# Optimization experiments

Measured on AMD Instinct MI355X. Metric: run time of the kernel, lower is better.

The kernel has to match this reference:

```python
import jax, jax.numpy as jnp
import numpy as np

MODEL_DIM = 1024
NUM_HEADS = 16
HEAD_DIM = MODEL_DIM // NUM_HEADS
EPS = 1e-12
CHUNK = 128  # chunk size for the linear-attention recurrence


def setup_inputs() -> dict:
    key = jax.random.key(0)
    kx, kq, kk, kv, ko = jax.random.split(key, 5)
    b, l = 4, 4096
    x = jax.random.normal(kx, (b, l, MODEL_DIM), dtype=jnp.float32)
    # nn.Linear weights, init std=0.02, no bias; torch Linear computes x @ W.T
    Wq = 0.02 * jax.random.normal(kq, (MODEL_DIM, MODEL_DIM), dtype=jnp.float32)
    Wk = 0.02 * jax.random.normal(kk, (MODEL_DIM, MODEL_DIM), dtype=jnp.float32)
    Wv = 0.02 * jax.random.normal(kv, (MODEL_DIM, MODEL_DIM), dtype=jnp.float32)
    Wo = 0.02 * jax.random.normal(ko, (MODEL_DIM, MODEL_DIM), dtype=jnp.float32)
    return {"x": x, "Wq": Wq, "Wk": Wk, "Wv": Wv, "Wo": Wo}


def _pos_elu(t):
    # feature_map = F.elu(x) + 1
    return jax.nn.elu(t) + 1.0


def _linear_attention(q, k, v):
    # q,k,v: (b,h,l,d) with feature map already applied.
    # Causal linear attention: out_t = (q_t . sum_{s<=t} k_s v_s^T) / (q_t . sum_{s<=t} k_s) + EPS
    # Chunked recurrence over the (d,d) KV state avoids the (b,h,l,d,d) cumsum.
    b, h, l, d = q.shape
    nc = l // CHUNK
    qc = jnp.moveaxis(q.reshape(b, h, nc, CHUNK, d), 2, 0)  # (nc,b,h,C,d)
    kc = jnp.moveaxis(k.reshape(b, h, nc, CHUNK, d), 2, 0)
    vc = jnp.moveaxis(v.reshape(b, h, nc, CHUNK, d), 2, 0)
    mask = jnp.tril(jnp.ones((CHUNK, CHUNK), dtype=q.dtype))  # causal within chunk

    def step(carry, inp):
        S, z = carry  # S:(b,h,d,d) running sum k v^T; z:(b,h,d) running sum k
        qb, kb, vb = inp  # (b,h,C,d)
        scores = jnp.einsum('bhcd,bhsd->bhcs', qb, kb) * mask  # (b,h,C,C)
        num = jnp.einsum('bhcd,bhde->bhce', qb, S) + jnp.einsum('bhcs,bhse->bhce', scores, vb)
        den = jnp.einsum('bhcd,bhd->bhc', qb, z) + scores.sum(-1)  # (b,h,C)
        out = num / den[..., None] + EPS  # NOTE: eps added after division, as in source
        S = S + jnp.einsum('bhsd,bhse->bhde', kb, vb)
        z = z + kb.sum(axis=2)
        return (S, z), out

    S0 = jnp.zeros((b, h, d, d), dtype=q.dtype)
    z0 = jnp.zeros((b, h, d), dtype=q.dtype)
    _, outs = jax.lax.scan(step, (S0, z0), (qc, kc, vc))  # (nc,b,h,C,d)
    # -> (b, l, h, d)
    return jnp.moveaxis(outs, 0, 1).transpose(0, 3, 1, 2, 4).reshape(b, h * 0 + l // l, 0, 0) if False else outs


def reference(x, Wq, Wk, Wv, Wo):
    b, l, D = x.shape
    h, d = NUM_HEADS, HEAD_DIM
    # projections (torch Linear: x @ W.T), split heads -> (b,h,l,d)
    q = (x @ Wq.T).reshape(b, l, h, d).transpose(0, 2, 1, 3)
    k = (x @ Wk.T).reshape(b, l, h, d).transpose(0, 2, 1, 3)
    v = (x @ Wv.T).reshape(b, l, h, d).transpose(0, 2, 1, 3)
    q = _pos_elu(q)
    k = _pos_elu(k)
    outs = _linear_attention(q, k, v)  # (nc,b,h,C,d)
    nc = l // CHUNK
    # (nc,b,h,C,d) -> (b,nc,C,h,d) -> (b,l,D)  (matches transpose(1,2).view in torch)
    attn = outs.transpose(1, 0, 3, 2, 4).reshape(b, l, D)
    return attn @ Wo.T
```

## Files before the change

### kernel.cpp

```cpp
#include <hip/hip_runtime.h>
#include <stdint.h>

typedef float f32x4 __attribute__((ext_vector_type(4)));
typedef __bf16 bf16x8 __attribute__((ext_vector_type(8)));
typedef unsigned short u16x8 __attribute__((ext_vector_type(8)));

#define DEV __device__ __forceinline__

DEV unsigned short f2bf(float f) {
  unsigned int u = __float_as_uint(f);
  unsigned int r = (u + 0x7FFFu + ((u >> 16) & 1u)) >> 16;
  return (unsigned short)r;
}
DEV float b2f(unsigned short h) { return __uint_as_float(((unsigned int)h) << 16); }

DEV void gload16(const void* g, void* l) {
  __builtin_amdgcn_global_load_lds((__attribute__((address_space(1))) void*)(g),
                                   (__attribute__((address_space(3))) void*)(l), 16, 0, 0);
}

__global__ void cast_bf16_kernel(const float* __restrict__ in,
                                 unsigned short* __restrict__ out, int n8) {
  int i = blockIdx.x * 256 + threadIdx.x;
  if (i >= n8) return;
  const float4* p = (const float4*)in + (size_t)i * 2;
  float4 a = p[0], b = p[1];
  u16x8 o;
  o[0] = f2bf(a.x); o[1] = f2bf(a.y); o[2] = f2bf(a.z); o[3] = f2bf(a.w);
  o[4] = f2bf(b.x); o[5] = f2bf(b.y); o[6] = f2bf(b.z); o[7] = f2bf(b.w);
  ((u16x8*)out)[i] = o;
}

__global__ void cast_w4(const float* __restrict__ Wq, const float* __restrict__ Wk,
                        const float* __restrict__ Wv, const float* __restrict__ Wo,
                        unsigned short* __restrict__ wqkv, unsigned short* __restrict__ wo) {
  int i = blockIdx.x * 256 + threadIdx.x;
  int sel = i >> 17, j = i & 131071;
  const float* src = (sel == 0) ? Wq : (sel == 1) ? Wk : (sel == 2) ? Wv : Wo;
  unsigned short* dst = (sel < 3) ? (wqkv + (size_t)sel * 1048576) : wo;
  const float4* p = (const float4*)src + (size_t)j * 2;
  float4 a = p[0], b = p[1];
  u16x8 o;
  o[0] = f2bf(a.x); o[1] = f2bf(a.y); o[2] = f2bf(a.z); o[3] = f2bf(a.w);
  o[4] = f2bf(b.x); o[5] = f2bf(b.y); o[6] = f2bf(b.z); o[7] = f2bf(b.w);
  ((u16x8*)dst)[j] = o;
}

template<int MODE>
__global__ __launch_bounds__(256, 2) void gemm_bt(
    const unsigned short* __restrict__ A, const unsigned short* __restrict__ Bw,
    void* __restrict__ out0, unsigned short* __restrict__ qp,
    unsigned short* __restrict__ kp, unsigned short* __restrict__ vp,
    int K, int N, int nTn)
{
  __shared__ unsigned short sA[128 * 64];
  __shared__ unsigned short sB[128 * 64];
  int t = threadIdx.x, w = t >> 6, lane = t & 63, fr = lane & 15, fq = lane >> 4;
  int nwg = gridDim.x, cpx = nwg >> 3;
  int bid = (blockIdx.x & 7) * cpx + (blockIdx.x >> 3);
  int bm = bid / nTn, bn = bid % nTn;
  int wm = w >> 1, wn = w & 1;

  f32x4 acc[4][4];
  f32x4 z4 = {0.f, 0.f, 0.f, 0.f};
#pragma unroll
  for (int mi = 0; mi < 4; ++mi)
#pragma unroll
    for (int ni = 0; ni < 4; ++ni) acc[mi][ni] = z4;

  for (int k0 = 0; k0 < K; k0 += 64) {
#pragma unroll
    for (int i = 0; i < 4; ++i) {
      int p = (i * 4 + w) * 64 + lane;
      int r = p >> 3;
      int c8 = (p & 7) ^ (r & 7);
      gload16(A + (size_t)(bm * 128 + r) * K + k0 + c8 * 8, &sA[(i * 4 + w) * 512]);
      gload16(Bw + (size_t)(bn * 128 + r) * K + k0 + c8 * 8, &sB[(i * 4 + w) * 512]);
    }
    __syncthreads();
#pragma unroll
    for (int ks = 0; ks < 2; ++ks) {
      bf16x8 af[4], bg[4];
#pragma unroll
      for (int mi = 0; mi < 4; ++mi) {
        int r = wm * 64 + mi * 16 + fr;
        int c8 = (ks * 4 + fq) ^ (r & 7);
        af[mi] = *(const bf16x8*)&sA[(r * 8 + c8) * 8];
      }
#pragma unroll
      for (int ni = 0; ni < 4; ++ni) {
        int r = wn * 64 + ni * 16 + fr;
        int c8 = (ks * 4 + fq) ^ (r & 7);
        bg[ni] = *(const bf16x8*)&sB[(r * 8 + c8) * 8];
      }
#pragma unroll
      for (int mi = 0; mi < 4; ++mi)
#pragma unroll
        for (int ni = 0; ni < 4; ++ni)
          acc[mi][ni] = __builtin_amdgcn_mfma_f32_16x16x32_bf16(af[mi], bg[ni], acc[mi][ni], 0, 0, 0);
    }
    __syncthreads();
  }

  if (MODE == 0) {
    float* O = (float*)out0;
#pragma unroll
    for (int mi = 0; mi < 4; ++mi)
#pragma unroll
      for (int ni = 0; ni < 4; ++ni)
#pragma unroll
        for (int j = 0; j < 4; ++j) {
          int m = bm * 128 + wm * 64 + mi * 16 + fq * 4 + j;
          int n = bn * 128 + wn * 64 + ni * 16 + fr;
          O[(size_t)m * N + n] = acc[mi][ni][j];
        }
  } else {
    int tsel = (bn * 128) >> 10;
    unsigned short* base = (tsel == 0) ? qp : ((tsel == 1) ? kp : vp);
#pragma unroll
    for (int mi = 0; mi < 4; ++mi)
#pragma unroll
      for (int ni = 0; ni < 4; ++ni)
#pragma unroll
        for (int j = 0; j < 4; ++j) {
          int m = bm * 128 + wm * 64 + mi * 16 + fq * 4 + j;
          int n = bn * 128 + wn * 64 + ni * 16 + fr;
          int col1 = n & 1023;
          int h = col1 >> 6, d = col1 & 63;
          int b = m >> 12, l = m & 4095;
          float v = acc[mi][ni][j];
          if (tsel < 2) v = (v > 0.f) ? (v + 1.f) : __expf(v);
          base[(((size_t)(b * 16 + h)) * 4096 + l) * 64 + d] = f2bf(v);
        }
  }
}

__global__ __launch_bounds__(256) void chunk_state(
    const unsigned short* __restrict__ kb, const unsigned short* __restrict__ vb,
    float* __restrict__ Sbuf, float* __restrict__ zbuf)
{
  __shared__ unsigned short kT[64 * 136];
  __shared__ unsigned short vT[64 * 136];
  int t = threadIdx.x, w = t >> 6, lane = t & 63, fr = lane & 15, fq = lane >> 4;
  int bh = blockIdx.x >> 5, c = blockIdx.x & 31;
  size_t base = ((size_t)bh * 4096 + (size_t)c * 128) * 64;

  int s = t >> 1, d0 = (t & 1) * 32;
  const unsigned short* kpp = kb + base + (size_t)s * 64 + d0;
  const unsigned short* vpp = vb + base + (size_t)s * 64 + d0;
#pragma unroll
  for (int i = 0; i < 4; ++i) {
    u16x8 kr = *(const u16x8*)(kpp + i * 8);
    u16x8 vr = *(const u16x8*)(vpp + i * 8);
#pragma unroll
    for (int j = 0; j < 8; ++j) {
      int d = d0 + i * 8 + j;
      kT[d * 136 + s] = kr[j];
      vT[d * 136 + s] = vr[j];
    }
  }
  __syncthreads();

  f32x4 acc[4];
  f32x4 z4 = {0.f, 0.f, 0.f, 0.f};
#pragma unroll
  for (int n = 0; n < 4; ++n) acc[n] = z4;
#pragma unroll
  for (int ks = 0; ks < 4; ++ks) {
    bf16x8 av = *(const bf16x8*)&vT[(w * 16 + fr) * 136 + ks * 32 + fq * 8];
#pragma unroll
    for (int n = 0; n < 4; ++n) {
      bf16x8 bk = *(const bf16x8*)&kT[(n * 16 + fr) * 136 + ks * 32 + fq * 8];
      acc[n] = __builtin_amdgcn_mfma_f32_16x16x32_bf16(av, bk, acc[n], 0, 0, 0);
    }
  }
  size_t ob = ((size_t)bh * 32 + c) * 4096;
#pragma unroll
  for (int n = 0; n < 4; ++n)
#pragma unroll
    for (int j = 0; j < 4; ++j) {
      int e = w * 16 + fq * 4 + j, d = n * 16 + fr;
      Sbuf[ob + (size_t)e * 64 + d] = acc[n][j];
    }
  if (t < 64) {
    float z = 0.f;
#pragma unroll
    for (int i = 0; i < 16; ++i) {
      u16x8 kr = *(const u16x8*)&kT[t * 136 + i * 8];
#pragma unroll
      for (int j = 0; j < 8; ++j) z += b2f(kr[j]);
    }
    zbuf[((size_t)bh * 32 + c) * 64 + t] = z;
  }
}

__global__ __launch_bounds__(256) void scan_S(
    const float* __restrict__ Sbuf, unsigned short* __restrict__ Spref)
{
  int idx = blockIdx.x * 256 + threadIdx.x;
  int bh = idx >> 12, i = idx & 4095;
  size_t base = (size_t)bh * 32 * 4096 + i;
  float run = 0.f;
#pragma unroll
  for (int c = 0; c < 32; ++c) {
    float v = Sbuf[base + (size_t)c * 4096];
    Spref[base + (size_t)c * 4096] = f2bf(run);
    run += v;
  }
}

__global__ __launch_bounds__(256) void scan_z(
    const float* __restrict__ zbuf, float* __restrict__ zpref)
{
  int idx = blockIdx.x * 256 + threadIdx.x;
  size_t base = (size_t)(idx >> 6) * 32 * 64 + (idx & 63);
  float run = 0.f;
#pragma unroll
  for (int c = 0; c < 32; ++c) {
    float v = zbuf[base + c * 64];
    zpref[base + c * 64] = run;
    run += v;
  }
}

__global__ __launch_bounds__(256, 2) void chunk_out(
    const unsigned short* __restrict__ qb, const unsigned short* __restrict__ kb,
    const unsigned short* __restrict__ vb, const unsigned short* __restrict__ Spref,
    const float* __restrict__ zpref, unsigned short* __restrict__ attn)
{
  __shared__ unsigned short sq[128 * 64];
  __shared__ unsigned short skv[128 * 64];
  __shared__ unsigned short ss[128 * 128];
  __shared__ unsigned short sS[80 * 64];
  int t = threadIdx.x, w = t >> 6, lane = t & 63, fr = lane & 15, fq = lane >> 4;
  int bh = blockIdx.x >> 5, c = blockIdx.x & 31;
  size_t qkbase = ((size_t)bh * 4096 + (size_t)c * 128) * 64;
  size_t sbase = ((size_t)bh * 32 + c) * 4096;

  u16x8 vreg[4];
#pragma unroll
  for (int i = 0; i < 4; ++i)
    vreg[i] = *(const u16x8*)(vb + qkbase + (size_t)(t * 4 + i) * 8);

#pragma unroll
  for (int i = 0; i < 4; ++i) {
    int p = t * 4 + i, r = p >> 3, c8 = p & 7;
    int sw = (r * 8 + (c8 ^ (r & 7))) * 8;
    *(u16x8*)&sq[sw] = *(const u16x8*)(qb + qkbase + (size_t)p * 8);
    *(u16x8*)&skv[sw] = *(const u16x8*)(kb + qkbase + (size_t)p * 8);
  }
#pragma unroll
  for (int i = 0; i < 2; ++i) {
    int p = t * 2 + i, e = p >> 3, c8 = p & 7;
    *(u16x8*)&sS[(e * 8 + (c8 ^ (e & 7))) * 8] = *(const u16x8*)(Spref + sbase + (size_t)p * 8);
  }
  if (t < 64) sS[64 * 64 + t] = f2bf(zpref[((size_t)bh * 32 + c) * 64 + t]);
  {
    unsigned int* zz = (unsigned int*)&sS[65 * 64];
    for (int i = t; i < 480; i += 256) zz[i] = 0u;
  }
  __syncthreads();

  int rowbase = w * 32;
  bf16x8 aq[2][2];
#pragma unroll
  for (int mi = 0; mi < 2; ++mi)
#pragma unroll
    for (int kt = 0; kt < 2; ++kt) {
      int r = rowbase + mi * 16 + fr;
      int c8 = (kt * 4 + fq) ^ (r & 7);
      aq[mi][kt] = *(const bf16x8*)&sq[(r * 8 + c8) * 8];
    }

  f32x4 accs[2][8];
  f32x4 z4 = {0.f, 0.f, 0.f, 0.f};
#pragma unroll
  for (int mi = 0; mi < 2; ++mi)
#pragma unroll
    for (int ni = 0; ni < 8; ++ni) accs[mi][ni] = z4;

#pragma unroll
  for (int ni = 0; ni < 8; ++ni)
#pragma unroll
    for (int kt = 0; kt < 2; ++kt) {
      int r = ni * 16 + fr;
      int c8 = (kt * 4 + fq) ^ (r & 7);
      bf16x8 bk = *(const bf16x8*)&skv[(r * 8 + c8) * 8];
      accs[0][ni] = __builtin_amdgcn_mfma_f32_16x16x32_bf16(aq[0][kt], bk, accs[0][ni], 0, 0, 0);
      accs[1][ni] = __builtin_amdgcn_mfma_f32_16x16x32_bf16(aq[1][kt], bk, accs[1][ni], 0, 0, 0);
    }

  float rs[2][4];
#pragma unroll
  for (int mi = 0; mi < 2; ++mi)
#pragma unroll
    for (int j = 0; j < 4; ++j) {
      int srow = rowbase + mi * 16 + fq * 4 + j;
      float sum = 0.f;
#pragma unroll
      for (int ni = 0; ni < 8; ++ni) {
        int scol = ni * 16 + fr;
        float v = accs[mi][ni][j];
        v = (scol <= srow) ? v : 0.f;
        accs[mi][ni][j] = v;
        sum += v;
      }
#pragma unroll
      for (int msk = 1; msk < 16; msk <<= 1) sum += __shfl_xor(sum, msk, 64);
      rs[mi][j] = sum;
    }
  __syncthreads();

#pragma unroll
  for (int i = 0; i < 4; ++i) {
    int p = t * 4 + i, s = p >> 3, e0g = (p & 7) * 8;
#pragma unroll
    for (int j = 0; j < 8; ++j) {
      int e = e0g + j;
      skv[(e * 16 + ((s >> 3) ^ (e & 15))) * 8 + (s & 7)] = vreg[i][j];
    }
  }
#pragma unroll
  for (int mi = 0; mi < 2; ++mi)
#pragma unroll
    for (int ni = 0; ni < 8; ++ni)
#pragma unroll
      for (int j = 0; j < 4; ++j) {
        int srow = rowbase + mi * 16 + fq * 4 + j;
        int scol = ni * 16 + fr;
        ss[(srow * 16 + ((scol >> 3) ^ (srow & 15))) * 8 + (scol & 7)] = f2bf(accs[mi][ni][j]);
      }
  __syncthreads();

  f32x4 acco[2][4];
  f32x4 accd[2];
#pragma unroll
  for (int mi = 0; mi < 2; ++mi) {
    accd[mi] = z4;
#pragma unroll
    for (int ni = 0; ni < 4; ++ni) acco[mi][ni] = z4;
  }
#pragma unroll
  for (int kt = 0; kt < 2; ++kt) {
#pragma unroll
    for (int ni = 0; ni < 4; ++ni) {
      int r = ni * 16 + fr;
      int c8 = (kt * 4 + fq) ^ (r & 7);
      bf16x8 bS = *(const bf16x8*)&sS[(r * 8 + c8) * 8];
      acco[0][ni] = __builtin_amdgcn_mfma_f32_16x16x32_bf16(aq[0][kt], bS, acco[0][ni], 0, 0, 0);
      acco[1][ni] = __builtin_amdgcn_mfma_f32_16x16x32_bf16(aq[1][kt], bS, acco[1][ni], 0, 0, 0);
    }
    {
      int r = 64 + fr;
      int c8 = (kt * 4 + fq) ^ (r & 7);
      bf16x8 bz = *(const bf16x8*)&sS[(r * 8 + c8) * 8];
      accd[0] = __builtin_amdgcn_mfma_f32_16x16x32_bf16(aq[0][kt], bz, accd[0], 0, 0, 0);
      accd[1] = __builtin_amdgcn_mfma_f32_16x16x32_bf16(aq[1][kt], bz, accd[1], 0, 0, 0);
    }
  }
#pragma unroll
  for (int kt = 0; kt < 4; ++kt) {
    bf16x8 am[2];
#pragma unroll
    for (int mi = 0; mi < 2; ++mi) {
      int r = rowbase + mi * 16 + fr;
      int c8 = (kt * 4 + fq) ^ (r & 15);
      am[mi] = *(const bf16x8*)&ss[(r * 16 + c8) * 8];
    }
#pragma unroll
    for (int ni = 0; ni < 4; ++ni) {
      int r = ni * 16 + fr;
      int c8 = (kt * 4 + fq) ^ (r & 15);
      bf16x8 bv = *(const bf16x8*)&skv[(r * 16 + c8) * 8];
      acco[0][ni] = __builtin_amdgcn_mfma_f32_16x16x32_bf16(am[0], bv, acco[0][ni], 0, 0, 0);
      acco[1][ni] = __builtin_amdgcn_mfma_f32_16x16x32_bf16(am[1], bv, acco[1][ni], 0, 0, 0);
    }
  }

  int b = bh >> 4, h = bh & 15;
#pragma unroll
  for (int mi = 0; mi < 2; ++mi)
#pragma unroll
    for (int j = 0; j < 4; ++j) {
      float den = __shfl(accd[mi][j], (lane & 48), 64) + rs[mi][j];
      float rden = 1.f / den;
      int m = rowbase + mi * 16 + fq * 4 + j;
      size_t rowoff = ((size_t)b * 4096 + (size_t)c * 128 + m) * 1024 + h * 64;
#pragma unroll
      for (int ni = 0; ni < 4; ++ni) {
        int e = ni * 16 + fr;
        float o = acco[mi][ni][j] * rden + 1e-12f;
        attn[rowoff + e] = f2bf(o);
      }
    }
}

extern "C" void kernel_launch(void* const* d_in, const int* in_sizes, int n_in,
                              void* d_out, int out_size, void* d_ws, size_t ws_size,
                              hipStream_t stream) {
  (void)in_sizes; (void)n_in; (void)out_size; (void)ws_size;
  const float* x = (const float*)d_in[0];
  const float* Wq = (const float*)d_in[1];
  const float* Wk = (const float*)d_in[2];
  const float* Wv = (const float*)d_in[3];
  const float* Wo = (const float*)d_in[4];
  char* ws = (char*)d_ws;
  unsigned short* xbf  = (unsigned short*)(ws + 0);
  unsigned short* wqkv = (unsigned short*)(ws + 33554432);
  unsigned short* wo   = (unsigned short*)(ws + 39845888);
  unsigned short* q    = (unsigned short*)(ws + 41943040);
  unsigned short* k    = (unsigned short*)(ws + 75497472);
  unsigned short* v    = (unsigned short*)(ws + 109051904);
  unsigned short* attn = (unsigned short*)(ws + 142606336);
  float* Sbuf          = (float*)(ws + 176160768);
  unsigned short* Spref= (unsigned short*)(ws + 209715200);
  float* zbuf          = (float*)(ws + 226492416);
  float* zpref         = (float*)(ws + 227016704);

  cast_bf16_kernel<<<8192, 256, 0, stream>>>(x, xbf, 2097152);
  cast_w4<<<2048, 256, 0, stream>>>(Wq, Wk, Wv, Wo, wqkv, wo);

  gemm_bt<1><<<3072, 256, 0, stream>>>(xbf, wqkv, nullptr, q, k, v, 1024, 3072, 24);
  chunk_state<<<2048, 256, 0, stream>>>(k, v, Sbuf, zbuf);
  scan_S<<<1024, 256, 0, stream>>>(Sbuf, Spref);
  scan_z<<<16, 256, 0, stream>>>(zbuf, zpref);
  chunk_out<<<2048, 256, 0, stream>>>(q, k, v, Spref, zpref, attn);
  gemm_bt<0><<<1024, 256, 0, stream>>>(attn, wo, d_out, nullptr, nullptr, nullptr, 1024, 1024, 8);
}
```

Baseline: 234.8 us.

## Merge cast and scan kernels, drop XCD remap, widen chunk_out to 512 threads

Fuses the two cast kernels into one launch and the two scan kernels into one launch to cut launch overhead. Removes the XCD-aware block remapping in the GEMM, so tiles are assigned in plain block order. Doubles chunk_out to 512 threads with 16 rows per wave instead of 32, which raises the wave count per block but halves per-wave MFMA work and register use. Dropping the remap may hurt L2 locality on the multi-XCD chip.

```diff
diff --git a/kernel.cpp b/kernel.cpp
--- a/kernel.cpp
+++ b/kernel.cpp
@@ -19,25 +19,22 @@
                                    (__attribute__((address_space(3))) void*)(l), 16, 0, 0);
 }
 
-__global__ void cast_bf16_kernel(const float* __restrict__ in,
-                                 unsigned short* __restrict__ out, int n8) {
+__global__ void cast_all(const float* __restrict__ x, const float* __restrict__ Wq,
+                         const float* __restrict__ Wk, const float* __restrict__ Wv,
+                         const float* __restrict__ Wo, unsigned short* __restrict__ xbf,
+                         unsigned short* __restrict__ wqkv, unsigned short* __restrict__ wo) {
   int i = blockIdx.x * 256 + threadIdx.x;
-  if (i >= n8) return;
-  const float4* p = (const float4*)in + (size_t)i * 2;
-  float4 a = p[0], b = p[1];
-  u16x8 o;
-  o[0] = f2bf(a.x); o[1] = f2bf(a.y); o[2] = f2bf(a.z); o[3] = f2bf(a.w);
-  o[4] = f2bf(b.x); o[5] = f2bf(b.y); o[6] = f2bf(b.z); o[7] = f2bf(b.w);
-  ((u16x8*)out)[i] = o;
-}
-
-__global__ void cast_w4(const float* __restrict__ Wq, const float* __restrict__ Wk,
-                        const float* __restrict__ Wv, const float* __restrict__ Wo,
-                        unsigned short* __restrict__ wqkv, unsigned short* __restrict__ wo) {
-  int i = blockIdx.x * 256 + threadIdx.x;
-  int sel = i >> 17, j = i & 131071;
-  const float* src = (sel == 0) ? Wq : (sel == 1) ? Wk : (sel == 2) ? Wv : Wo;
-  unsigned short* dst = (sel < 3) ? (wqkv + (size_t)sel * 1048576) : wo;
+  const float* src;
+  unsigned short* dst;
+  int j;
+  if (i < 2097152) {
+    src = x; dst = xbf; j = i;
+  } else {
+    int k = i - 2097152;
+    int sel = k >> 17; j = k & 131071;
+    src = (sel == 0) ? Wq : (sel == 1) ? Wk : (sel == 2) ? Wv : Wo;
+    dst = (sel < 3) ? (wqkv + (size_t)sel * 1048576) : wo;
+  }
   const float4* p = (const float4*)src + (size_t)j * 2;
   float4 a = p[0], b = p[1];
   u16x8 o;
@@ -56,8 +53,7 @@
   __shared__ unsigned short sA[128 * 64];
   __shared__ unsigned short sB[128 * 64];
   int t = threadIdx.x, w = t >> 6, lane = t & 63, fr = lane & 15, fq = lane >> 4;
-  int nwg = gridDim.x, cpx = nwg >> 3;
-  int bid = (blockIdx.x & 7) * cpx + (blockIdx.x >> 3);
+  int bid = blockIdx.x;
   int bm = bid / nTn, bn = bid % nTn;
   int wm = w >> 1, wn = w & 1;
 
@@ -194,36 +190,35 @@
   }
 }
 
-__global__ __launch_bounds__(256) void scan_S(
-    const float* __restrict__ Sbuf, unsigned short* __restrict__ Spref)
+__global__ __launch_bounds__(256) void scan_all(
+    const float* __restrict__ Sbuf, const float* __restrict__ zbuf,
+    unsigned short* __restrict__ Spref, float* __restrict__ zpref)
 {
-  int idx = blockIdx.x * 256 + threadIdx.x;
-  int bh = idx >> 12, i = idx & 4095;
-  size_t base = (size_t)bh * 32 * 4096 + i;
-  float run = 0.f;
-#pragma unroll
-  for (int c = 0; c < 32; ++c) {
-    float v = Sbuf[base + (size_t)c * 4096];
-    Spref[base + (size_t)c * 4096] = f2bf(run);
-    run += v;
-  }
-}
-
-__global__ __launch_bounds__(256) void scan_z(
-    const float* __restrict__ zbuf, float* __restrict__ zpref)
-{
-  int idx = blockIdx.x * 256 + threadIdx.x;
-  size_t base = (size_t)(idx >> 6) * 32 * 64 + (idx & 63);
-  float run = 0.f;
-#pragma unroll
-  for (int c = 0; c < 32; ++c) {
-    float v = zbuf[base + c * 64];
-    zpref[base + c * 64] = run;
-    run += v;
-  }
-}
-
-__global__ __launch_bounds__(256, 2) void chunk_out(
+  if (blockIdx.x < 1024) {
+    int idx = blockIdx.x * 256 + threadIdx.x;
+    int bh = idx >> 12, i = idx & 4095;
+    size_t base = (size_t)bh * 32 * 4096 + i;
+    float run = 0.f;
+#pragma unroll
+    for (int c = 0; c < 32; ++c) {
+      float v = Sbuf[base + (size_t)c * 4096];
+      Spref[base + (size_t)c * 4096] = f2bf(run);
+      run += v;
+    }
+  } else {
+    int idx = (blockIdx.x - 1024) * 256 + threadIdx.x;
+    size_t base = (size_t)(idx >> 6) * 32 * 64 + (idx & 63);
+    float run = 0.f;
+#pragma unroll
+    for (int c = 0; c < 32; ++c) {
+      float v = zbuf[base + c * 64];
+      zpref[base + c * 64] = run;
+      run += v;
+    }
+  }
+}
+
+__global__ __launch_bounds__(512, 2) void chunk_out(
     const unsigned short* __restrict__ qb, const unsigned short* __restrict__ kb,
     const unsigned short* __restrict__ vb, const unsigned short* __restrict__ Spref,
     const float* __restrict__ zpref, unsigned short* __restrict__ attn)
@@ -237,47 +232,42 @@
   size_t qkbase = ((size_t)bh * 4096 + (size_t)c * 128) * 64;
   size_t sbase = ((size_t)bh * 32 + c) * 4096;
 
-  u16x8 vreg[4];
-#pragma unroll
-  for (int i = 0; i < 4; ++i)
-    vreg[i] = *(const u16x8*)(vb + qkbase + (size_t)(t * 4 + i) * 8);
-
-#pragma unroll
-  for (int i = 0; i < 4; ++i) {
-    int p = t * 4 + i, r = p >> 3, c8 = p & 7;
+  u16x8 vreg[2];
+#pragma unroll
+  for (int i = 0; i < 2; ++i)
+    vreg[i] = *(const u16x8*)(vb + qkbase + (size_t)(t * 2 + i) * 8);
+
+#pragma unroll
+  for (int i = 0; i < 2; ++i) {
+    int p = t * 2 + i, r = p >> 3, c8 = p & 7;
     int sw = (r * 8 + (c8 ^ (r & 7))) * 8;
     *(u16x8*)&sq[sw] = *(const u16x8*)(qb + qkbase + (size_t)p * 8);
     *(u16x8*)&skv[sw] = *(const u16x8*)(kb + qkbase + (size_t)p * 8);
   }
-#pragma unroll
-  for (int i = 0; i < 2; ++i) {
-    int p = t * 2 + i, e = p >> 3, c8 = p & 7;
+  {
+    int p = t, e = p >> 3, c8 = p & 7;
     *(u16x8*)&sS[(e * 8 + (c8 ^ (e & 7))) * 8] = *(const u16x8*)(Spref + sbase + (size_t)p * 8);
   }
   if (t < 64) sS[64 * 64 + t] = f2bf(zpref[((size_t)bh * 32 + c) * 64 + t]);
   {
     unsigned int* zz = (unsigned int*)&sS[65 * 64];
-    for (int i = t; i < 480; i += 256) zz[i] = 0u;
+    for (int i = t; i < 480; i += 512) zz[i] = 0u;
   }
   __syncthreads();
 
-  int rowbase = w * 32;
-  bf16x8 aq[2][2];
-#pragma unroll
-  for (int mi = 0; mi < 2; ++mi)
-#pragma unroll
-    for (int kt = 0; kt < 2; ++kt) {
-      int r = rowbase + mi * 16 + fr;
-      int c8 = (kt * 4 + fq) ^ (r & 7);
-      aq[mi][kt] = *(const bf16x8*)&sq[(r * 8 + c8) * 8];
-    }
-
-  f32x4 accs[2][8];
+  int rowbase = w * 16;
+  bf16x8 aq[2];
+#pragma unroll
+  for (int kt = 0; kt < 2; ++kt) {
+    int r = rowbase + fr;
+    int c8 = (kt * 4 + fq) ^ (r & 7);
+    aq[kt] = *(const bf16x8*)&sq[(r * 8 + c8) * 8];
+  }
+
+  f32x4 accs[8];
   f32x4 z4 = {0.f, 0.f, 0.f, 0.f};
 #pragma unroll
-  for (int mi = 0; mi < 2; ++mi)
-#pragma unroll
-    for (int ni = 0; ni < 8; ++ni) accs[mi][ni] = z4;
+  for (int ni = 0; ni < 8; ++ni) accs[ni] = z4;
 
 #pragma unroll
   for (int ni = 0; ni < 8; ++ni)
@@ -286,34 +276,31 @@
       int r = ni * 16 + fr;
       int c8 = (kt * 4 + fq) ^ (r & 7);
       bf16x8 bk = *(const bf16x8*)&skv[(r * 8 + c8) * 8];
-      accs[0][ni] = __builtin_amdgcn_mfma_f32_16x16x32_bf16(aq[0][kt], bk, accs[0][ni], 0, 0, 0);
-      accs[1][ni] = __builtin_amdgcn_mfma_f32_16x16x32_bf16(aq[1][kt], bk, accs[1][ni], 0, 0, 0);
-    }
-
-  float rs[2][4];
-#pragma unroll
-  for (int mi = 0; mi < 2; ++mi)
-#pragma unroll
-    for (int j = 0; j < 4; ++j) {
-      int srow = rowbase + mi * 16 + fq * 4 + j;
-      float sum = 0.f;
-#pragma unroll
-      for (int ni = 0; ni < 8; ++ni) {
-        int scol = ni * 16 + fr;
-        float v = accs[mi][ni][j];
-        v = (scol <= srow) ? v : 0.f;
-        accs[mi][ni][j] = v;
-        sum += v;
-      }
-#pragma unroll
-      for (int msk = 1; msk < 16; msk <<= 1) sum += __shfl_xor(sum, msk, 64);
-      rs[mi][j] = sum;
-    }
+      accs[ni] = __builtin_amdgcn_mfma_f32_16x16x32_bf16(aq[kt], bk, accs[ni], 0, 0, 0);
+    }
+
+  float rs[4];
+#pragma unroll
+  for (int j = 0; j < 4; ++j) {
+    int srow = rowbase + fq * 4 + j;
+    float sum = 0.f;
+#pragma unroll
+    for (int ni = 0; ni < 8; ++ni) {
+      int scol = ni * 16 + fr;
+      float v = accs[ni][j];
+      v = (scol <= srow) ? v : 0.f;
+      accs[ni][j] = v;
+      sum += v;
+    }
+#pragma unroll
+    for (int msk = 1; msk < 16; msk <<= 1) sum += __shfl_xor(sum, msk, 64);
+    rs[j] = sum;
+  }
   __syncthreads();
 
 #pragma unroll
-  for (int i = 0; i < 4; ++i) {
-    int p = t * 4 + i, s = p >> 3, e0g = (p & 7) * 8;
+  for (int i = 0; i < 2; ++i) {
+    int p = t * 2 + i, s = p >> 3, e0g = (p & 7) * 8;
 #pragma unroll
     for (int j = 0; j < 8; ++j) {
       int e = e0g + j;
@@ -321,25 +308,20 @@
     }
   }
 #pragma unroll
-  for (int mi = 0; mi < 2; ++mi)
-#pragma unroll
-    for (int ni = 0; ni < 8; ++ni)
-#pragma unroll
-      for (int j = 0; j < 4; ++j) {
-        int srow = rowbase + mi * 16 + fq * 4 + j;
-        int scol = ni * 16 + fr;
-        ss[(srow * 16 + ((scol >> 3) ^ (srow & 15))) * 8 + (scol & 7)] = f2bf(accs[mi][ni][j]);
-      }
+  for (int ni = 0; ni < 8; ++ni)
+#pragma unroll
+    for (int j = 0; j < 4; ++j) {
+      int srow = rowbase + fq * 4 + j;
+      int scol = ni * 16 + fr;
+      ss[(srow * 16 + ((scol >> 3) ^ (srow & 15))) * 8 + (scol & 7)] = f2bf(accs[ni][j]);
+    }
   __syncthreads();
 
-  f32x4 acco[2][4];
-  f32x4 accd[2];
-#pragma unroll
-  for (int mi = 0; mi < 2; ++mi) {
-    accd[mi] = z4;
-#pragma unroll
-    for (int ni = 0; ni < 4; ++ni) acco[mi][ni] = z4;
-  }
+  f32x4 acco[4];
+  f32x4 accd = z4;
+#pragma unroll
+  for (int ni = 0; ni < 4; ++ni) acco[ni] = z4;
+
 #pragma unroll
   for (int kt = 0; kt < 2; ++kt) {
 #pragma unroll
@@ -347,52 +329,46 @@
       int r = ni * 16 + fr;
       int c8 = (kt * 4 + fq) ^ (r & 7);
       bf16x8 bS = *(const bf16x8*)&sS[(r * 8 + c8) * 8];
-      acco[0][ni] = __builtin_amdgcn_mfma_f32_16x16x32_bf16(aq[0][kt], bS, acco[0][ni], 0, 0, 0);
-      acco[1][ni] = __builtin_amdgcn_mfma_f32_16x16x32_bf16(aq[1][kt], bS, acco[1][ni], 0, 0, 0);
+      acco[ni] = __builtin_amdgcn_mfma_f32_16x16x32_bf16(aq[kt], bS, acco[ni], 0, 0, 0);
     }
     {
       int r = 64 + fr;
       int c8 = (kt * 4 + fq) ^ (r & 7);
       bf16x8 bz = *(const bf16x8*)&sS[(r * 8 + c8) * 8];
-      accd[0] = __builtin_amdgcn_mfma_f32_16x16x32_bf16(aq[0][kt], bz, accd[0], 0, 0, 0);
-      accd[1] = __builtin_amdgcn_mfma_f32_16x16x32_bf16(aq[1][kt], bz, accd[1], 0, 0, 0);
+      accd = __builtin_amdgcn_mfma_f32_16x16x32_bf16(aq[kt], bz, accd, 0, 0, 0);
     }
   }
 #pragma unroll
   for (int kt = 0; kt < 4; ++kt) {
-    bf16x8 am[2];
-#pragma unroll
-    for (int mi = 0; mi < 2; ++mi) {
-      int r = rowbase + mi * 16 + fr;
+    bf16x8 am;
+    {
+      int r = rowbase + fr;
       int c8 = (kt * 4 + fq) ^ (r & 15);
-      am[mi] = *(const bf16x8*)&ss[(r * 16 + c8) * 8];
+      am = *(const bf16x8*)&ss[(r * 16 + c8) * 8];
     }
 #pragma unroll
     for (int ni = 0; ni < 4; ++ni) {
       int r = ni * 16 + fr;
       int c8 = (kt * 4 + fq) ^ (r & 15);
       bf16x8 bv = *(const bf16x8*)&skv[(r * 16 + c8) * 8];
-      acco[0][ni] = __builtin_amdgcn_mfma_f32_16x16x32_bf16(am[0], bv, acco[0][ni], 0, 0, 0);
-      acco[1][ni] = __builtin_amdgcn_mfma_f32_16x16x32_bf16(am[1], bv, acco[1][ni], 0, 0, 0);
+      acco[ni] = __builtin_amdgcn_mfma_f32_16x16x32_bf16(am, bv, acco[ni], 0, 0, 0);
     }
   }
 
   int b = bh >> 4, h = bh & 15;
 #pragma unroll
-  for (int mi = 0; mi < 2; ++mi)
-#pragma unroll
-    for (int j = 0; j < 4; ++j) {
-      float den = __shfl(accd[mi][j], (lane & 48), 64) + rs[mi][j];
-      float rden = 1.f / den;
-      int m = rowbase + mi * 16 + fq * 4 + j;
-      size_t rowoff = ((size_t)b * 4096 + (size_t)c * 128 + m) * 1024 + h * 64;
-#pragma unroll
-      for (int ni = 0; ni < 4; ++ni) {
-        int e = ni * 16 + fr;
-        float o = acco[mi][ni][j] * rden + 1e-12f;
-        attn[rowoff + e] = f2bf(o);
-      }
-    }
+  for (int j = 0; j < 4; ++j) {
+    float den = __shfl(accd[j], (lane & 48), 64) + rs[j];
+    float rden = 1.f / den;
+    int m = rowbase + fq * 4 + j;
+    size_t rowoff = ((size_t)b * 4096 + (size_t)c * 128 + m) * 1024 + h * 64;
+#pragma unroll
+    for (int ni = 0; ni < 4; ++ni) {
+      int e = ni * 16 + fr;
+      float o = acco[ni][j] * rden + 1e-12f;
+      attn[rowoff + e] = f2bf(o);
+    }
+  }
 }
 
 extern "C" void kernel_launch(void* const* d_in, const int* in_sizes, int n_in,
@@ -417,13 +393,10 @@
   float* zbuf          = (float*)(ws + 226492416);
   float* zpref         = (float*)(ws + 227016704);
 
-  cast_bf16_kernel<<<8192, 256, 0, stream>>>(x, xbf, 2097152);
-  cast_w4<<<2048, 256, 0, stream>>>(Wq, Wk, Wv, Wo, wqkv, wo);
-
+  cast_all<<<10240, 256, 0, stream>>>(x, Wq, Wk, Wv, Wo, xbf, wqkv, wo);
   gemm_bt<1><<<3072, 256, 0, stream>>>(xbf, wqkv, nullptr, q, k, v, 1024, 3072, 24);
   chunk_state<<<2048, 256, 0, stream>>>(k, v, Sbuf, zbuf);
-  scan_S<<<1024, 256, 0, stream>>>(Sbuf, Spref);
-  scan_z<<<16, 256, 0, stream>>>(zbuf, zpref);
-  chunk_out<<<2048, 256, 0, stream>>>(q, k, v, Spref, zpref, attn);
+  scan_all<<<1040, 256, 0, stream>>>(Sbuf, zbuf, Spref, zpref);
+  chunk_out<<<2048, 512, 0, stream>>>(q, k, v, Spref, zpref, attn);
   gemm_bt<0><<<1024, 256, 0, stream>>>(attn, wo, d_out, nullptr, nullptr, nullptr, 1024, 1024, 8);
 }
```

Result: slower. 242.9 us (+3.5%).

## Merge cast and scan kernels, transpose score MFMA, drop GEMM block swizzle

Applied to the files above, without the earlier changes.

Merges the two cast kernels into one launch and the two prefix-scan kernels into one, cutting launch count. It removes the XCD-aware block remapping in the GEMM so blocks map linearly. chunk_state now loads K/V column-wise per lane so its LDS transposed stores are vectorized. chunk_out computes the score tile transposed so the causal mask, row sums and packed 32-bit LDS stores need fewer shuffles and scalar stores. Dropping the swizzle may reduce L2 locality on the multi-XCD GPU, and the strided global loads in chunk_state may coalesce worse.

```diff
diff --git a/kernel.cpp b/kernel.cpp
--- a/kernel.cpp
+++ b/kernel.cpp
@@ -19,25 +19,22 @@
                                    (__attribute__((address_space(3))) void*)(l), 16, 0, 0);
 }
 
-__global__ void cast_bf16_kernel(const float* __restrict__ in,
-                                 unsigned short* __restrict__ out, int n8) {
+__global__ void cast_all(const float* __restrict__ x, const float* __restrict__ Wq,
+                         const float* __restrict__ Wk, const float* __restrict__ Wv,
+                         const float* __restrict__ Wo, unsigned short* __restrict__ xbf,
+                         unsigned short* __restrict__ wqkv, unsigned short* __restrict__ wo) {
   int i = blockIdx.x * 256 + threadIdx.x;
-  if (i >= n8) return;
-  const float4* p = (const float4*)in + (size_t)i * 2;
-  float4 a = p[0], b = p[1];
-  u16x8 o;
-  o[0] = f2bf(a.x); o[1] = f2bf(a.y); o[2] = f2bf(a.z); o[3] = f2bf(a.w);
-  o[4] = f2bf(b.x); o[5] = f2bf(b.y); o[6] = f2bf(b.z); o[7] = f2bf(b.w);
-  ((u16x8*)out)[i] = o;
-}
-
-__global__ void cast_w4(const float* __restrict__ Wq, const float* __restrict__ Wk,
-                        const float* __restrict__ Wv, const float* __restrict__ Wo,
-                        unsigned short* __restrict__ wqkv, unsigned short* __restrict__ wo) {
-  int i = blockIdx.x * 256 + threadIdx.x;
-  int sel = i >> 17, j = i & 131071;
-  const float* src = (sel == 0) ? Wq : (sel == 1) ? Wk : (sel == 2) ? Wv : Wo;
-  unsigned short* dst = (sel < 3) ? (wqkv + (size_t)sel * 1048576) : wo;
+  const float* src;
+  unsigned short* dst;
+  int j;
+  if (i < 2097152) {
+    src = x; dst = xbf; j = i;
+  } else {
+    int k = i - 2097152;
+    int sel = k >> 17; j = k & 131071;
+    src = (sel == 0) ? Wq : (sel == 1) ? Wk : (sel == 2) ? Wv : Wo;
+    dst = (sel < 3) ? (wqkv + (size_t)sel * 1048576) : wo;
+  }
   const float4* p = (const float4*)src + (size_t)j * 2;
   float4 a = p[0], b = p[1];
   u16x8 o;
@@ -56,8 +53,7 @@
   __shared__ unsigned short sA[128 * 64];
   __shared__ unsigned short sB[128 * 64];
   int t = threadIdx.x, w = t >> 6, lane = t & 63, fr = lane & 15, fq = lane >> 4;
-  int nwg = gridDim.x, cpx = nwg >> 3;
-  int bid = (blockIdx.x & 7) * cpx + (blockIdx.x >> 3);
+  int bid = blockIdx.x;
   int bm = bid / nTn, bn = bid % nTn;
   int wm = w >> 1, wn = w & 1;
 
@@ -145,19 +141,19 @@
   int bh = blockIdx.x >> 5, c = blockIdx.x & 31;
   size_t base = ((size_t)bh * 4096 + (size_t)c * 128) * 64;
 
-  int s = t >> 1, d0 = (t & 1) * 32;
-  const unsigned short* kpp = kb + base + (size_t)s * 64 + d0;
-  const unsigned short* vpp = vb + base + (size_t)s * 64 + d0;
-#pragma unroll
-  for (int i = 0; i < 4; ++i) {
-    u16x8 kr = *(const u16x8*)(kpp + i * 8);
-    u16x8 vr = *(const u16x8*)(vpp + i * 8);
-#pragma unroll
-    for (int j = 0; j < 8; ++j) {
-      int d = d0 + i * 8 + j;
-      kT[d * 136 + s] = kr[j];
-      vT[d * 136 + s] = vr[j];
-    }
+  int d = lane;
+  int s0 = w * 8;
+#pragma unroll
+  for (int c4 = 0; c4 < 4; ++c4) {
+    int sb = c4 * 32 + s0;
+    u16x8 kr, vr;
+#pragma unroll
+    for (int i = 0; i < 8; ++i) {
+      kr[i] = kb[base + (size_t)(sb + i) * 64 + d];
+      vr[i] = vb[base + (size_t)(sb + i) * 64 + d];
+    }
+    *(u16x8*)&kT[d * 136 + sb] = kr;
+    *(u16x8*)&vT[d * 136 + sb] = vr;
   }
   __syncthreads();
 
@@ -179,8 +175,8 @@
   for (int n = 0; n < 4; ++n)
 #pragma unroll
     for (int j = 0; j < 4; ++j) {
-      int e = w * 16 + fq * 4 + j, d = n * 16 + fr;
-      Sbuf[ob + (size_t)e * 64 + d] = acc[n][j];
+      int e = w * 16 + fq * 4 + j, dd = n * 16 + fr;
+      Sbuf[ob + (size_t)e * 64 + dd] = acc[n][j];
     }
   if (t < 64) {
     float z = 0.f;
@@ -194,32 +190,31 @@
   }
 }
 
-__global__ __launch_bounds__(256) void scan_S(
-    const float* __restrict__ Sbuf, unsigned short* __restrict__ Spref)
+__global__ __launch_bounds__(256) void scan_all(
+    const float* __restrict__ Sbuf, const float* __restrict__ zbuf,
+    unsigned short* __restrict__ Spref, float* __restrict__ zpref)
 {
-  int idx = blockIdx.x * 256 + threadIdx.x;
-  int bh = idx >> 12, i = idx & 4095;
-  size_t base = (size_t)bh * 32 * 4096 + i;
-  float run = 0.f;
-#pragma unroll
-  for (int c = 0; c < 32; ++c) {
-    float v = Sbuf[base + (size_t)c * 4096];
-    Spref[base + (size_t)c * 4096] = f2bf(run);
-    run += v;
-  }
-}
-
-__global__ __launch_bounds__(256) void scan_z(
-    const float* __restrict__ zbuf, float* __restrict__ zpref)
-{
-  int idx = blockIdx.x * 256 + threadIdx.x;
-  size_t base = (size_t)(idx >> 6) * 32 * 64 + (idx & 63);
-  float run = 0.f;
-#pragma unroll
-  for (int c = 0; c < 32; ++c) {
-    float v = zbuf[base + c * 64];
-    zpref[base + c * 64] = run;
-    run += v;
+  if (blockIdx.x < 1024) {
+    int idx = blockIdx.x * 256 + threadIdx.x;
+    int bh = idx >> 12, i = idx & 4095;
+    size_t base = (size_t)bh * 32 * 4096 + i;
+    float run = 0.f;
+#pragma unroll
+    for (int c = 0; c < 32; ++c) {
+      float v = Sbuf[base + (size_t)c * 4096];
+      Spref[base + (size_t)c * 4096] = f2bf(run);
+      run += v;
+    }
+  } else {
+    int idx = (blockIdx.x - 1024) * 256 + threadIdx.x;
+    size_t base = (size_t)(idx >> 6) * 32 * 64 + (idx & 63);
+    float run = 0.f;
+#pragma unroll
+    for (int c = 0; c < 32; ++c) {
+      float v = zbuf[base + c * 64];
+      zpref[base + c * 64] = run;
+      run += v;
+    }
   }
 }
 
@@ -272,12 +267,12 @@
       aq[mi][kt] = *(const bf16x8*)&sq[(r * 8 + c8) * 8];
     }
 
-  f32x4 accs[2][8];
+  f32x4 accsT[2][8];
   f32x4 z4 = {0.f, 0.f, 0.f, 0.f};
 #pragma unroll
   for (int mi = 0; mi < 2; ++mi)
 #pragma unroll
-    for (int ni = 0; ni < 8; ++ni) accs[mi][ni] = z4;
+    for (int ni = 0; ni < 8; ++ni) accsT[mi][ni] = z4;
 
 #pragma unroll
   for (int ni = 0; ni < 8; ++ni)
@@ -286,29 +281,28 @@
       int r = ni * 16 + fr;
       int c8 = (kt * 4 + fq) ^ (r & 7);
       bf16x8 bk = *(const bf16x8*)&skv[(r * 8 + c8) * 8];
-      accs[0][ni] = __builtin_amdgcn_mfma_f32_16x16x32_bf16(aq[0][kt], bk, accs[0][ni], 0, 0, 0);
-      accs[1][ni] = __builtin_amdgcn_mfma_f32_16x16x32_bf16(aq[1][kt], bk, accs[1][ni], 0, 0, 0);
-    }
-
-  float rs[2][4];
-#pragma unroll
-  for (int mi = 0; mi < 2; ++mi)
-#pragma unroll
-    for (int j = 0; j < 4; ++j) {
-      int srow = rowbase + mi * 16 + fq * 4 + j;
-      float sum = 0.f;
-#pragma unroll
-      for (int ni = 0; ni < 8; ++ni) {
-        int scol = ni * 16 + fr;
-        float v = accs[mi][ni][j];
-        v = (scol <= srow) ? v : 0.f;
-        accs[mi][ni][j] = v;
+      accsT[0][ni] = __builtin_amdgcn_mfma_f32_16x16x32_bf16(bk, aq[0][kt], accsT[0][ni], 0, 0, 0);
+      accsT[1][ni] = __builtin_amdgcn_mfma_f32_16x16x32_bf16(bk, aq[1][kt], accsT[1][ni], 0, 0, 0);
+    }
+
+  float rs[2];
+#pragma unroll
+  for (int mi = 0; mi < 2; ++mi) {
+    int m16 = mi * 16 + fr;
+    float sum = 0.f;
+#pragma unroll
+    for (int ni = 0; ni < 8; ++ni)
+#pragma unroll
+      for (int j = 0; j < 4; ++j) {
+        int s = ni * 16 + fq * 4 + j - rowbase;
+        float v = (s <= m16) ? accsT[mi][ni][j] : 0.f;
+        accsT[mi][ni][j] = v;
         sum += v;
       }
-#pragma unroll
-      for (int msk = 1; msk < 16; msk <<= 1) sum += __shfl_xor(sum, msk, 64);
-      rs[mi][j] = sum;
-    }
+    sum += __shfl_xor(sum, 16, 64);
+    sum += __shfl_xor(sum, 32, 64);
+    rs[mi] = sum;
+  }
   __syncthreads();
 
 #pragma unroll
@@ -321,15 +315,18 @@
     }
   }
 #pragma unroll
-  for (int mi = 0; mi < 2; ++mi)
+  for (int mi = 0; mi < 2; ++mi) {
+    int m = rowbase + mi * 16 + fr;
 #pragma unroll
     for (int ni = 0; ni < 8; ++ni)
 #pragma unroll
-      for (int j = 0; j < 4; ++j) {
-        int srow = rowbase + mi * 16 + fq * 4 + j;
-        int scol = ni * 16 + fr;
-        ss[(srow * 16 + ((scol >> 3) ^ (srow & 15))) * 8 + (scol & 7)] = f2bf(accs[mi][ni][j]);
+      for (int p = 0; p < 2; ++p) {
+        unsigned int pk = (unsigned int)f2bf(accsT[mi][ni][2 * p]) |
+                          ((unsigned int)f2bf(accsT[mi][ni][2 * p + 1]) << 16);
+        int chunk = (2 * ni + (fq >> 1)) ^ (m & 15);
+        *(unsigned int*)&ss[m * 128 + chunk * 8 + (fq & 1) * 4 + 2 * p] = pk;
       }
+  }
   __syncthreads();
 
   f32x4 acco[2][4];
@@ -382,7 +379,8 @@
   for (int mi = 0; mi < 2; ++mi)
 #pragma unroll
     for (int j = 0; j < 4; ++j) {
-      float den = __shfl(accd[mi][j], (lane & 48), 64) + rs[mi][j];
+      float rsj = __shfl(rs[mi], fq * 4 + j, 64);
+      float den = __shfl(accd[mi][j], (lane & 48), 64) + rsj;
       float rden = 1.f / den;
       int m = rowbase + mi * 16 + fq * 4 + j;
       size_t rowoff = ((size_t)b * 4096 + (size_t)c * 128 + m) * 1024 + h * 64;
@@ -417,13 +415,10 @@
   float* zbuf          = (float*)(ws + 226492416);
   float* zpref         = (float*)(ws + 227016704);
 
-  cast_bf16_kernel<<<8192, 256, 0, stream>>>(x, xbf, 2097152);
-  cast_w4<<<2048, 256, 0, stream>>>(Wq, Wk, Wv, Wo, wqkv, wo);
-
+  cast_all<<<10240, 256, 0, stream>>>(x, Wq, Wk, Wv, Wo, xbf, wqkv, wo);
   gemm_bt<1><<<3072, 256, 0, stream>>>(xbf, wqkv, nullptr, q, k, v, 1024, 3072, 24);
   chunk_state<<<2048, 256, 0, stream>>>(k, v, Sbuf, zbuf);
-  scan_S<<<1024, 256, 0, stream>>>(Sbuf, Spref);
-  scan_z<<<16, 256, 0, stream>>>(zbuf, zpref);
+  scan_all<<<1040, 256, 0, stream>>>(Sbuf, zbuf, Spref, zpref);
   chunk_out<<<2048, 256, 0, stream>>>(q, k, v, Spref, zpref, attn);
   gemm_bt<0><<<1024, 256, 0, stream>>>(attn, wo, d_out, nullptr, nullptr, nullptr, 1024, 1024, 8);
 }
```

Result: slower. 242.0 us (+3.1%).
